# Kernel optimization log

Hardware: AMD Instinct MI355X
Metric: run time of the kernel (lower is better)

## Reference

```python
import jax, jax.numpy as jnp
import numpy as np

N = 50000      # nodes
E = 800000     # edges (before self-loops)
DIN = 64
DH = 64
DOUT = 64
G = 500        # graphs in batch
EPS = 1e-5     # BatchNorm eps


def setup_inputs() -> dict:
    key = jax.random.key(0)
    ks = jax.random.split(key, 8)
    x = jax.random.normal(ks[0], (N, DIN), dtype=jnp.float32)
    edge_index = jax.random.randint(ks[1], (2, E), 0, N, dtype=jnp.int32)
    batch = jnp.sort(jax.random.randint(ks[2], (N,), 0, G, dtype=jnp.int32))

    def lin(k, di, do):
        return (jax.random.normal(k, (di, do), dtype=jnp.float32) / np.float32(np.sqrt(di)))

    inp = dict(x=x, edge_index=edge_index, batch=batch)
    dims = [(DIN, DH), (DH, DH), (DH, DOUT)]
    for i, (di, do) in enumerate(dims, start=1):
        inp[f"W{i}"] = lin(ks[2 + i], di, do)
        inp[f"b{i}"] = jnp.zeros((do,), jnp.float32)
        inp[f"gamma{i}"] = jnp.ones((do,), jnp.float32)
        inp[f"beta{i}"] = jnp.zeros((do,), jnp.float32)
    return inp


def _gcn_norm(edge_index, n_nodes):
    # add self loops, compute symmetric normalization deg^-1/2 * deg^-1/2
    loop = jnp.arange(n_nodes, dtype=edge_index.dtype)
    src = jnp.concatenate([edge_index[0], loop])
    dst = jnp.concatenate([edge_index[1], loop])
    deg = jax.ops.segment_sum(jnp.ones_like(dst, dtype=jnp.float32), dst,
                              num_segments=n_nodes)
    dinv = jax.lax.rsqrt(deg)  # deg >= 1 thanks to self-loops
    norm = dinv[src] * dinv[dst]  # [E + N]
    return src, dst, norm


def _gcn_conv(x, src, dst, norm, W, b, n_nodes):
    h = x @ W                               # [N, dout]
    msg = h[src] * norm[:, None]            # gather + scale  [E+N, dout]
    out = jax.ops.segment_sum(msg, dst, num_segments=n_nodes)  # scatter-add
    return out + b


def _batchnorm(x, gamma, beta):
    mean = jnp.mean(x, axis=0)
    var = jnp.mean(jnp.square(x - mean), axis=0)  # biased, as in torch training BN
    return gamma * (x - mean) * jax.lax.rsqrt(var + EPS) + beta


def reference(x, edge_index, batch, W1, b1, gamma1, beta1,
              W2, b2, gamma2, beta2, W3, b3, gamma3, beta3):
    src, dst, norm = _gcn_norm(edge_index, N)
    layers = [(W1, b1, gamma1, beta1), (W2, b2, gamma2, beta2),
              (W3, b3, gamma3, beta3)]
    h = x
    for i, (W, b, g, be) in enumerate(layers):
        h = _gcn_conv(h, src, dst, norm, W, b, N)
        h = _batchnorm(h, g, be)
        if i < len(layers) - 1:
            h = jax.nn.relu(h)  # dropout is identity in eval / reference
    # global mean pool over graphs
    sums = jax.ops.segment_sum(h, batch, num_segments=G)          # [G, DOUT]
    cnts = jax.ops.segment_sum(jnp.ones((N,), jnp.float32), batch,
                               num_segments=G)
    return sums / jnp.maximum(cnts, 1.0)[:, None]
```

## Files before the change

### kernel.cpp

```cpp
#include <hip/hip_runtime.h>
#include <hip/hip_fp16.h>

#define BN_EPS 1e-5f
#define CCH 4096
#define NSLICE 32
#define OUT_CAP 8192
#define CAP 8192
#define SXS 68


__device__ inline __half2 u2h(unsigned u) {
    union { unsigned u; __half2 h; } x; x.u = u; return x.h;
}
__device__ inline unsigned h2u(__half2 h) {
    union { unsigned u; __half2 h; } x; x.h = h; return x.u;
}
__device__ inline unsigned pack_f16x2(float a, float b) {
    return h2u(__floats2half2_rn(a, b));
}


__global__ __launch_bounds__(256) void scatter_direct(const int* __restrict__ src,
                                                      const int* __restrict__ dst,
                                                      int* __restrict__ ccnt,
                                                      unsigned* __restrict__ tmp,
                                                      float* __restrict__ cnt_g,
                                                      float* __restrict__ out,
                                                      int E, int G) {
    __shared__ int lcnt[256];
    int t = threadIdx.x;
    int tid = blockIdx.x * 256 + t;
    int stride = gridDim.x * 256;
    for (int i = tid; i < G * 64; i += stride) out[i] = 0.f;
    for (int i = tid; i < G; i += stride) cnt_g[i] = 0.f;

    int e0 = blockIdx.x * CCH;
    lcnt[t] = 0;
    __syncthreads();
#pragma unroll
    for (int k = 0; k < CCH / 256; ++k) {
        int e = e0 + k * 256 + t;
        if (e < E) atomicAdd(&lcnt[dst[e] >> 8], 1);
    }
    __syncthreads();
    int c = lcnt[t];
    __syncthreads();
    if (c > 0) lcnt[t] = t * CAP + atomicAdd(&ccnt[t], c);
    __syncthreads();
#pragma unroll
    for (int k = 0; k < CCH / 256; ++k) {
        int e = e0 + k * 256 + t;
        if (e < E) {
            int d = dst[e];
            int pos = atomicAdd(&lcnt[d >> 8], 1);
            tmp[pos] = ((unsigned)src[e] << 8) | (unsigned)(d & 255);
        }
    }
}


__global__ __launch_bounds__(256) void build_csr(const unsigned* __restrict__ tmp,
                                                 const int* __restrict__ ccnt,
                                                 int* __restrict__ rp,
                                                 unsigned short* __restrict__ deg,
                                                 unsigned short* __restrict__ col,
                                                 float* __restrict__ dinv,
                                                 const int* __restrict__ batch,
                                                 float* __restrict__ cnt_g,
                                                 int n, int G) {
    __shared__ int hist[256];
    __shared__ int sc[256];
    __shared__ unsigned short outw[OUT_CAP];
    __shared__ int h[512];
    int b = blockIdx.x;
    int t = threadIdx.x;
    int beg = b * CAP;
    int m = ccnt[b];
    int end = beg + m;
    hist[t] = 0;
    __syncthreads();
    for (int e = beg + t; e < end; e += 256) atomicAdd(&hist[tmp[e] & 255u], 1);
    __syncthreads();
    int v = hist[t];
    sc[t] = v;
    __syncthreads();
    for (int off = 1; off < 256; off <<= 1) {
        int u = (t >= off) ? sc[t - off] : 0;
        __syncthreads();
        sc[t] += u;
        __syncthreads();
    }
    int excl = sc[t] - v;
    int node = b * 256 + t;
    if (node < n) {
        dinv[node] = rsqrtf(1.0f + (float)v);
        rp[node] = beg + excl;
        deg[node] = (unsigned short)v;
    }
    hist[t] = excl;
    __syncthreads();
    if (m <= OUT_CAP) {
        for (int e = beg + t; e < end; e += 256) {
            unsigned p = tmp[e];
            int pos = atomicAdd(&hist[p & 255u], 1);
            outw[pos] = (unsigned short)(p >> 8);
        }
        __syncthreads();
        for (int i = t; i < m; i += 256) col[beg + i] = outw[i];
    } else {
        for (int e = beg + t; e < end; e += 256) {
            unsigned p = tmp[e];
            int pos = atomicAdd(&hist[p & 255u], 1);
            col[beg + pos] = (unsigned short)(p >> 8);
        }
    }
    if (G <= 512) {
        __syncthreads();
        for (int i = t; i < 512; i += 256) h[i] = 0;
        __syncthreads();
        for (int i = b * 256 + t; i < n; i += gridDim.x * 256)
            atomicAdd(&h[batch[i]], 1);
        __syncthreads();
        for (int i = t; i < G; i += 256)
            if (h[i]) atomicAdd(&cnt_g[i], (float)h[i]);
    } else {
        for (int i = b * 256 + t; i < n; i += gridDim.x * 256)
            atomicAdd(&cnt_g[batch[i]], 1.0f);
    }
}


__global__ __launch_bounds__(256) void gemm64_v2(const float* __restrict__ X,
                                                 const float* __restrict__ W,
                                                 const float* __restrict__ dinv,
                                                 const float* __restrict__ part,
                                                 const float* __restrict__ gamma,
                                                 const float* __restrict__ beta,
                                                 int has_bn, float inv_n,
                                                 unsigned* __restrict__ Hs, int n) {
    __shared__ float sX[64 * SXS];
    __shared__ float sW[64 * SXS];
    __shared__ float s_scsh[128];
    int t = threadIdx.x;
    int c4 = t & 15;
    int base = blockIdx.x * 64;

    if (has_bn) {
        if (t < 128) {
            float s = 0.f;
#pragma unroll
            for (int k = 0; k < NSLICE; ++k) s += part[k * 128 + t];
            s_scsh[t] = s;
        }
        __syncthreads();
        if (t < 64) {
            float mean = s_scsh[t] * inv_n;
            float var = s_scsh[64 + t] * inv_n - mean * mean;
            float sc = gamma[t] * rsqrtf(var + BN_EPS);
            s_scsh[t] = sc;
            s_scsh[64 + t] = beta[t] - mean * sc;
        }
        __syncthreads();
    }

    {
        const float4* W4 = (const float4*)W;
#pragma unroll
        for (int it = 0; it < 4; ++it) {
            int idx = it * 256 + t;
            int r = idx >> 4;
            float4 v = W4[r * 16 + c4];
            *(float4*)&sW[r * SXS + c4 * 4] = v;
        }
    }
    {
        const float4* X4 = (const float4*)X;
        float4 sc4, sh4;
        if (has_bn) {
            sc4 = *(const float4*)&s_scsh[c4 * 4];
            sh4 = *(const float4*)&s_scsh[64 + c4 * 4];
        }
#pragma unroll
        for (int it = 0; it < 4; ++it) {
            int idx = it * 256 + t;
            int r = idx >> 4;
            int grow = base + r;
            float4 v = make_float4(0.f, 0.f, 0.f, 0.f);
            if (grow < n) v = X4[(size_t)grow * 16 + c4];
            if (has_bn) {
                v.x = fmaxf(fmaf(v.x, sc4.x, sh4.x), 0.f);
                v.y = fmaxf(fmaf(v.y, sc4.y, sh4.y), 0.f);
                v.z = fmaxf(fmaf(v.z, sc4.z, sh4.z), 0.f);
                v.w = fmaxf(fmaf(v.w, sc4.w, sh4.w), 0.f);
            }
            *(float4*)&sX[r * SXS + c4 * 4] = v;
        }
    }
    __syncthreads();

    int rgrp = t >> 4;
    float4 acc[4];
#pragma unroll
    for (int ri = 0; ri < 4; ++ri) acc[ri] = make_float4(0.f, 0.f, 0.f, 0.f);

#pragma unroll 4
    for (int k4 = 0; k4 < 16; ++k4) {
        float4 xv[4], wv[4];
#pragma unroll
        for (int ri = 0; ri < 4; ++ri)
            xv[ri] = *(const float4*)&sX[(rgrp + 16 * ri) * SXS + k4 * 4];
#pragma unroll
        for (int kk = 0; kk < 4; ++kk)
            wv[kk] = *(const float4*)&sW[(k4 * 4 + kk) * SXS + c4 * 4];
#pragma unroll
        for (int ri = 0; ri < 4; ++ri) {
            acc[ri].x = fmaf(xv[ri].x, wv[0].x, acc[ri].x);
            acc[ri].y = fmaf(xv[ri].x, wv[0].y, acc[ri].y);
            acc[ri].z = fmaf(xv[ri].x, wv[0].z, acc[ri].z);
            acc[ri].w = fmaf(xv[ri].x, wv[0].w, acc[ri].w);
            acc[ri].x = fmaf(xv[ri].y, wv[1].x, acc[ri].x);
            acc[ri].y = fmaf(xv[ri].y, wv[1].y, acc[ri].y);
            acc[ri].z = fmaf(xv[ri].y, wv[1].z, acc[ri].z);
            acc[ri].w = fmaf(xv[ri].y, wv[1].w, acc[ri].w);
            acc[ri].x = fmaf(xv[ri].z, wv[2].x, acc[ri].x);
            acc[ri].y = fmaf(xv[ri].z, wv[2].y, acc[ri].y);
            acc[ri].z = fmaf(xv[ri].z, wv[2].z, acc[ri].z);
            acc[ri].w = fmaf(xv[ri].z, wv[2].w, acc[ri].w);
            acc[ri].x = fmaf(xv[ri].w, wv[3].x, acc[ri].x);
            acc[ri].y = fmaf(xv[ri].w, wv[3].y, acc[ri].y);
            acc[ri].z = fmaf(xv[ri].w, wv[3].z, acc[ri].z);
            acc[ri].w = fmaf(xv[ri].w, wv[3].w, acc[ri].w);
        }
    }

#pragma unroll
    for (int ri = 0; ri < 4; ++ri) {
        int row = base + rgrp + 16 * ri;
        if (row < n) {
            float dv = dinv[row];
            uint2 o2;
            o2.x = pack_f16x2(acc[ri].x * dv, acc[ri].y * dv);
            o2.y = pack_f16x2(acc[ri].z * dv, acc[ri].w * dv);
            ((uint2*)Hs)[(size_t)row * 16 + c4] = o2;
        }
    }
}


__global__ __launch_bounds__(256) void agg(const uint4* __restrict__ Hs4,
                                           const int* __restrict__ rp,
                                           const unsigned short* __restrict__ deg,
                                           const unsigned short* __restrict__ col,
                                           const float* __restrict__ dinv,
                                           float* __restrict__ Y,
                                           float* __restrict__ part, int n) {
    __shared__ float sS[8][64];
    __shared__ float sQ[8][64];
    int t = threadIdx.x;
    int w = t >> 6;
    int lane = t & 63;
    int h = lane >> 5;
    int l5 = lane & 31;
    int g4 = l5 >> 3;
    int c = l5 & 7;
    int d = blockIdx.x * 8 + w * 2 + h;
    bool valid = d < n;
    int dc = valid ? d : 0;
    __half2 a0 = u2h(0u), a1 = u2h(0u), a2 = u2h(0u), a3 = u2h(0u);
    int beg = 0, end = 0;
    if (valid) { beg = rp[dc]; end = beg + (int)deg[dc]; }
    for (int b = beg; b < end; b += 32) {
        int m = min(32, end - b);
        int myidx = (l5 < m) ? (int)col[b + l5] : 0;
        uint4 v[8];
#pragma unroll
        for (int k = 0; k < 8; ++k) {
            int e = 4 * k + g4;
            int s0 = __shfl(myidx, e, 32);
            if (e < m) v[k] = Hs4[(size_t)s0 * 8 + c];
        }
#pragma unroll
        for (int k = 0; k < 8; ++k) {
            int e = 4 * k + g4;
            if (e < m) {
                a0 = __hadd2(a0, u2h(v[k].x)); a1 = __hadd2(a1, u2h(v[k].y));
                a2 = __hadd2(a2, u2h(v[k].z)); a3 = __hadd2(a3, u2h(v[k].w));
            }
        }
    }
#pragma unroll
    for (int mask = 8; mask <= 16; mask <<= 1) {
        a0 = __hadd2(a0, u2h((unsigned)__shfl_xor((int)h2u(a0), mask, 64)));
        a1 = __hadd2(a1, u2h((unsigned)__shfl_xor((int)h2u(a1), mask, 64)));
        a2 = __hadd2(a2, u2h((unsigned)__shfl_xor((int)h2u(a2), mask, 64)));
        a3 = __hadd2(a3, u2h((unsigned)__shfl_xor((int)h2u(a3), mask, 64)));
    }
    if (g4 == 0) {
        float2 f0 = __half22float2(a0), f1 = __half22float2(a1);
        float2 f2 = __half22float2(a2), f3 = __half22float2(a3);
        float y0 = f0.x, y1 = f0.y, y2 = f1.x, y3 = f1.y;
        float y4 = f2.x, y5 = f2.y, y6 = f3.x, y7 = f3.y;
        if (valid) {
            uint4 hv = Hs4[(size_t)dc * 8 + c];
            float2 h0 = __half22float2(u2h(hv.x)), h1 = __half22float2(u2h(hv.y));
            float2 h2v = __half22float2(u2h(hv.z)), h3 = __half22float2(u2h(hv.w));
            float dv = dinv[dc];
            y0 = (y0 + h0.x) * dv; y1 = (y1 + h0.y) * dv;
            y2 = (y2 + h1.x) * dv; y3 = (y3 + h1.y) * dv;
            y4 = (y4 + h2v.x) * dv; y5 = (y5 + h2v.y) * dv;
            y6 = (y6 + h3.x) * dv; y7 = (y7 + h3.y) * dv;
            *(float4*)&Y[(size_t)dc * 64 + c * 8]     = make_float4(y0, y1, y2, y3);
            *(float4*)&Y[(size_t)dc * 64 + c * 8 + 4] = make_float4(y4, y5, y6, y7);
        } else {
            y0 = y1 = y2 = y3 = y4 = y5 = y6 = y7 = 0.f;
        }
        int slot = w * 2 + h;
        *(float4*)&sS[slot][c * 8]     = make_float4(y0, y1, y2, y3);
        *(float4*)&sS[slot][c * 8 + 4] = make_float4(y4, y5, y6, y7);
        *(float4*)&sQ[slot][c * 8]     = make_float4(y0 * y0, y1 * y1, y2 * y2, y3 * y3);
        *(float4*)&sQ[slot][c * 8 + 4] = make_float4(y4 * y4, y5 * y5, y6 * y6, y7 * y7);
    }
    __syncthreads();
    if (t < 64) {
        float s = 0.f, qq = 0.f;
#pragma unroll
        for (int i = 0; i < 8; ++i) { s += sS[i][t]; qq += sQ[i][t]; }
        float* dst = part + (size_t)(blockIdx.x & (NSLICE - 1)) * 128;
        atomicAdd(&dst[t], s);
        atomicAdd(&dst[64 + t], qq);
    }
}

__global__ __launch_bounds__(256) void agg_pool(const uint4* __restrict__ Hs4,
                                                const int* __restrict__ rp,
                                                const unsigned short* __restrict__ deg,
                                                const unsigned short* __restrict__ col,
                                                const float* __restrict__ dinv,
                                                const int* __restrict__ batch,
                                                float* __restrict__ out,
                                                float* __restrict__ part, int n) {
    __shared__ float sS[8][64];
    __shared__ float sQ[8][64];
    __shared__ int sG[8];
    int t = threadIdx.x;
    int w = t >> 6;
    int lane = t & 63;
    int h = lane >> 5;
    int l5 = lane & 31;
    int g4 = l5 >> 3;
    int c = l5 & 7;
    int d = blockIdx.x * 8 + w * 2 + h;
    bool valid = d < n;
    int dc = valid ? d : 0;
    __half2 a0 = u2h(0u), a1 = u2h(0u), a2 = u2h(0u), a3 = u2h(0u);
    int beg = 0, end = 0;
    if (valid) { beg = rp[dc]; end = beg + (int)deg[dc]; }
    for (int b = beg; b < end; b += 32) {
        int m = min(32, end - b);
        int myidx = (l5 < m) ? (int)col[b + l5] : 0;
        uint4 v[8];
#pragma unroll
        for (int k = 0; k < 8; ++k) {
            int e = 4 * k + g4;
            int s0 = __shfl(myidx, e, 32);
            if (e < m) v[k] = Hs4[(size_t)s0 * 8 + c];
        }
#pragma unroll
        for (int k = 0; k < 8; ++k) {
            int e = 4 * k + g4;
            if (e < m) {
                a0 = __hadd2(a0, u2h(v[k].x)); a1 = __hadd2(a1, u2h(v[k].y));
                a2 = __hadd2(a2, u2h(v[k].z)); a3 = __hadd2(a3, u2h(v[k].w));
            }
        }
    }
#pragma unroll
    for (int mask = 8; mask <= 16; mask <<= 1) {
        a0 = __hadd2(a0, u2h((unsigned)__shfl_xor((int)h2u(a0), mask, 64)));
        a1 = __hadd2(a1, u2h((unsigned)__shfl_xor((int)h2u(a1), mask, 64)));
        a2 = __hadd2(a2, u2h((unsigned)__shfl_xor((int)h2u(a2), mask, 64)));
        a3 = __hadd2(a3, u2h((unsigned)__shfl_xor((int)h2u(a3), mask, 64)));
    }
    if (g4 == 0) {
        float2 f0 = __half22float2(a0), f1 = __half22float2(a1);
        float2 f2 = __half22float2(a2), f3 = __half22float2(a3);
        float y0 = f0.x, y1 = f0.y, y2 = f1.x, y3 = f1.y;
        float y4 = f2.x, y5 = f2.y, y6 = f3.x, y7 = f3.y;
        if (valid) {
            uint4 hv = Hs4[(size_t)dc * 8 + c];
            float2 h0 = __half22float2(u2h(hv.x)), h1 = __half22float2(u2h(hv.y));
            float2 h2v = __half22float2(u2h(hv.z)), h3 = __half22float2(u2h(hv.w));
            float dv = dinv[dc];
            y0 = (y0 + h0.x) * dv; y1 = (y1 + h0.y) * dv;
            y2 = (y2 + h1.x) * dv; y3 = (y3 + h1.y) * dv;
            y4 = (y4 + h2v.x) * dv; y5 = (y5 + h2v.y) * dv;
            y6 = (y6 + h3.x) * dv; y7 = (y7 + h3.y) * dv;
        } else {
            y0 = y1 = y2 = y3 = y4 = y5 = y6 = y7 = 0.f;
        }
        int slot = w * 2 + h;
        *(float4*)&sS[slot][c * 8]     = make_float4(y0, y1, y2, y3);
        *(float4*)&sS[slot][c * 8 + 4] = make_float4(y4, y5, y6, y7);
        *(float4*)&sQ[slot][c * 8]     = make_float4(y0 * y0, y1 * y1, y2 * y2, y3 * y3);
        *(float4*)&sQ[slot][c * 8 + 4] = make_float4(y4 * y4, y5 * y5, y6 * y6, y7 * y7);
        if (l5 == 0) sG[slot] = valid ? batch[dc] : -1;
    }
    __syncthreads();
    if (t < 64) {
        float s = 0.f, qq = 0.f;
#pragma unroll
        for (int i = 0; i < 8; ++i) { s += sS[i][t]; qq += sQ[i][t]; }
        float* dst = part + (size_t)(blockIdx.x & (NSLICE - 1)) * 128;
        atomicAdd(&dst[t], s);
        atomicAdd(&dst[64 + t], qq);
        int g0 = sG[0];
        bool same = (g0 >= 0);
#pragma unroll
        for (int i = 1; i < 8; ++i) same = same && (sG[i] == g0);
        if (same) {
            atomicAdd(&out[(size_t)g0 * 64 + t], s);
        } else {
#pragma unroll
            for (int i = 0; i < 8; ++i) {
                int gi = sG[i];
                if (gi >= 0) atomicAdd(&out[(size_t)gi * 64 + t], sS[i][t]);
            }
        }
    }
}


__global__ __launch_bounds__(256) void pool_div(float* __restrict__ out,
                                                const float* __restrict__ cnt,
                                                const float* __restrict__ part,
                                                const float* __restrict__ gamma,
                                                const float* __restrict__ beta,
                                                int G, float inv_n) {
    __shared__ float s_scsh[128];
    int t = threadIdx.x;
    if (t < 128) {
        float s = 0.f;
#pragma unroll
        for (int k = 0; k < NSLICE; ++k) s += part[k * 128 + t];
        s_scsh[t] = s;
    }
    __syncthreads();
    if (t < 64) {
        float mean = s_scsh[t] * inv_n;
        float var = s_scsh[64 + t] * inv_n - mean * mean;
        float sc = gamma[t] * rsqrtf(var + BN_EPS);
        s_scsh[t] = sc;
        s_scsh[64 + t] = beta[t] - mean * sc;
    }
    __syncthreads();
    int idx = blockIdx.x * 256 + t;
    if (idx >= G * 64) return;
    int j = idx & 63, g = idx >> 6;
    float c = cnt[g];
    out[idx] = (c > 0.5f) ? fmaf(s_scsh[j], out[idx] / c, s_scsh[64 + j]) : 0.f;
}


extern "C" void kernel_launch(void* const* d_in, const int* in_sizes, int n_in,
                              void* d_out, int out_size, void* d_ws, size_t ws_size,
                              hipStream_t stream) {
    const float* x     = (const float*)d_in[0];
    const int*   ei    = (const int*)d_in[1];
    const int*   batch = (const int*)d_in[2];
    const float* Wl[3] = {(const float*)d_in[3], (const float*)d_in[7], (const float*)d_in[11]};
    const float* gl[3] = {(const float*)d_in[5], (const float*)d_in[9], (const float*)d_in[13]};
    const float* bl[3] = {(const float*)d_in[6], (const float*)d_in[10], (const float*)d_in[14]};
    float* out = (float*)d_out;

    int E = in_sizes[1] / 2;
    int n = in_sizes[0] / 64;
    int G = out_size / 64;
    const int* src = ei;
    const int* dst = ei + E;
    int NBC = (n + 255) / 256;
    float inv_n = 1.0f / (float)n;

    char* ws = (char*)d_ws;
    size_t off = 0;
    auto carve = [&](size_t bytes) {
        void* p = ws + off;
        off += (bytes + 255) & ~(size_t)255;
        return p;
    };
    float*          part  = (float*)carve(3 * NSLICE * 128 * 4);
    int*            ccnt  = (int*)carve(256 * 4);
    float*          dinv  = (float*)carve((size_t)n * 4);
    float*          cnt_g = (float*)carve((size_t)G * 4);
    unsigned*       Hs    = (unsigned*)carve((size_t)n * 32 * 4);
    float*          Ybuf  = (float*)carve((size_t)n * 64 * 4);
    int*            rp    = (int*)carve(((size_t)n + 1) * 4);
    unsigned short* deg   = (unsigned short*)carve((size_t)n * 2);
    unsigned*       tmp   = (unsigned*)carve((size_t)NBC * CAP * 4);
    unsigned short* col   = (unsigned short*)carve((size_t)NBC * CAP * 2);

    int pgrid = (E + CCH - 1) / CCH;
    int gemm_grid = (n + 63) / 64;
    int agg_grid = (n + 7) / 8;

    hipMemsetAsync(part, 0, 3 * NSLICE * 128 * 4 + 256 * 4, stream);
    scatter_direct<<<pgrid, 256, 0, stream>>>(src, dst, ccnt, tmp, cnt_g, out, E, G);
    build_csr<<<NBC, 256, 0, stream>>>(tmp, ccnt, rp, deg, col, dinv, batch, cnt_g, n, G);

    const float* cur = x;
    for (int l = 0; l < 3; ++l) {
        float* part_l = part + (size_t)l * NSLICE * 128;
        const float* part_prev = (l > 0) ? part + (size_t)(l - 1) * NSLICE * 128 : part;
        gemm64_v2<<<gemm_grid, 256, 0, stream>>>(cur, Wl[l], dinv, part_prev,
                                                 l > 0 ? gl[l - 1] : gl[0],
                                                 l > 0 ? bl[l - 1] : bl[0],
                                                 l > 0 ? 1 : 0, inv_n, Hs, n);
        if (l < 2) {
            agg<<<agg_grid, 256, 0, stream>>>((const uint4*)Hs, rp, deg, col, dinv,
                                              Ybuf, part_l, n);
        } else {
            agg_pool<<<agg_grid, 256, 0, stream>>>((const uint4*)Hs, rp, deg, col, dinv,
                                                   batch, out, part_l, n);
        }
        cur = Ybuf;
    }

    pool_div<<<(G * 64 + 255) / 256, 256, 0, stream>>>(out, cnt_g,
                                                       part + 2 * NSLICE * 128,
                                                       gl[2], bl[2], G, inv_n);
}
```

Before: 229.1 us.

## Assign one 8-lane group per destination node in aggregation kernels

```diff
diff --git a/kernel.cpp b/kernel.cpp
--- a/kernel.cpp
+++ b/kernel.cpp
@@ -254,77 +254,64 @@
                                            const float* __restrict__ dinv,
                                            float* __restrict__ Y,
                                            float* __restrict__ part, int n) {
-    __shared__ float sS[8][64];
-    __shared__ float sQ[8][64];
+    __shared__ float sS[32][64];
+    __shared__ float sQ[32][64];
     int t = threadIdx.x;
     int w = t >> 6;
     int lane = t & 63;
-    int h = lane >> 5;
-    int l5 = lane & 31;
-    int g4 = l5 >> 3;
-    int c = l5 & 7;
-    int d = blockIdx.x * 8 + w * 2 + h;
+    int dslot = lane >> 3;
+    int c = lane & 7;
+    int slot = w * 8 + dslot;
+    int d = blockIdx.x * 32 + slot;
     bool valid = d < n;
     int dc = valid ? d : 0;
     __half2 a0 = u2h(0u), a1 = u2h(0u), a2 = u2h(0u), a3 = u2h(0u);
     int beg = 0, end = 0;
     if (valid) { beg = rp[dc]; end = beg + (int)deg[dc]; }
-    for (int b = beg; b < end; b += 32) {
-        int m = min(32, end - b);
-        int myidx = (l5 < m) ? (int)col[b + l5] : 0;
+    for (int b = beg; b < end; b += 8) {
+        int m = min(8, end - b);
+        int myidx = (c < m) ? (int)col[b + c] : 0;
         uint4 v[8];
 #pragma unroll
         for (int k = 0; k < 8; ++k) {
-            int e = 4 * k + g4;
-            int s0 = __shfl(myidx, e, 32);
-            if (e < m) v[k] = Hs4[(size_t)s0 * 8 + c];
+            int s0 = __shfl(myidx, k, 8);
+            if (k < m) v[k] = Hs4[(size_t)s0 * 8 + c];
         }
 #pragma unroll
         for (int k = 0; k < 8; ++k) {
-            int e = 4 * k + g4;
-            if (e < m) {
+            if (k < m) {
                 a0 = __hadd2(a0, u2h(v[k].x)); a1 = __hadd2(a1, u2h(v[k].y));
                 a2 = __hadd2(a2, u2h(v[k].z)); a3 = __hadd2(a3, u2h(v[k].w));
             }
         }
     }
-#pragma unroll
-    for (int mask = 8; mask <= 16; mask <<= 1) {
-        a0 = __hadd2(a0, u2h((unsigned)__shfl_xor((int)h2u(a0), mask, 64)));
-        a1 = __hadd2(a1, u2h((unsigned)__shfl_xor((int)h2u(a1), mask, 64)));
-        a2 = __hadd2(a2, u2h((unsigned)__shfl_xor((int)h2u(a2), mask, 64)));
-        a3 = __hadd2(a3, u2h((unsigned)__shfl_xor((int)h2u(a3), mask, 64)));
-    }
-    if (g4 == 0) {
-        float2 f0 = __half22float2(a0), f1 = __half22float2(a1);
-        float2 f2 = __half22float2(a2), f3 = __half22float2(a3);
-        float y0 = f0.x, y1 = f0.y, y2 = f1.x, y3 = f1.y;
-        float y4 = f2.x, y5 = f2.y, y6 = f3.x, y7 = f3.y;
-        if (valid) {
-            uint4 hv = Hs4[(size_t)dc * 8 + c];
-            float2 h0 = __half22float2(u2h(hv.x)), h1 = __half22float2(u2h(hv.y));
-            float2 h2v = __half22float2(u2h(hv.z)), h3 = __half22float2(u2h(hv.w));
-            float dv = dinv[dc];
-            y0 = (y0 + h0.x) * dv; y1 = (y1 + h0.y) * dv;
-            y2 = (y2 + h1.x) * dv; y3 = (y3 + h1.y) * dv;
-            y4 = (y4 + h2v.x) * dv; y5 = (y5 + h2v.y) * dv;
-            y6 = (y6 + h3.x) * dv; y7 = (y7 + h3.y) * dv;
-            *(float4*)&Y[(size_t)dc * 64 + c * 8]     = make_float4(y0, y1, y2, y3);
-            *(float4*)&Y[(size_t)dc * 64 + c * 8 + 4] = make_float4(y4, y5, y6, y7);
-        } else {
-            y0 = y1 = y2 = y3 = y4 = y5 = y6 = y7 = 0.f;
-        }
-        int slot = w * 2 + h;
-        *(float4*)&sS[slot][c * 8]     = make_float4(y0, y1, y2, y3);
-        *(float4*)&sS[slot][c * 8 + 4] = make_float4(y4, y5, y6, y7);
-        *(float4*)&sQ[slot][c * 8]     = make_float4(y0 * y0, y1 * y1, y2 * y2, y3 * y3);
-        *(float4*)&sQ[slot][c * 8 + 4] = make_float4(y4 * y4, y5 * y5, y6 * y6, y7 * y7);
-    }
+    float2 f0 = __half22float2(a0), f1 = __half22float2(a1);
+    float2 f2 = __half22float2(a2), f3 = __half22float2(a3);
+    float y0 = f0.x, y1 = f0.y, y2 = f1.x, y3 = f1.y;
+    float y4 = f2.x, y5 = f2.y, y6 = f3.x, y7 = f3.y;
+    if (valid) {
+        uint4 hv = Hs4[(size_t)dc * 8 + c];
+        float2 h0 = __half22float2(u2h(hv.x)), h1 = __half22float2(u2h(hv.y));
+        float2 h2v = __half22float2(u2h(hv.z)), h3 = __half22float2(u2h(hv.w));
+        float dv = dinv[dc];
+        y0 = (y0 + h0.x) * dv; y1 = (y1 + h0.y) * dv;
+        y2 = (y2 + h1.x) * dv; y3 = (y3 + h1.y) * dv;
+        y4 = (y4 + h2v.x) * dv; y5 = (y5 + h2v.y) * dv;
+        y6 = (y6 + h3.x) * dv; y7 = (y7 + h3.y) * dv;
+        *(float4*)&Y[(size_t)dc * 64 + c * 8]     = make_float4(y0, y1, y2, y3);
+        *(float4*)&Y[(size_t)dc * 64 + c * 8 + 4] = make_float4(y4, y5, y6, y7);
+    } else {
+        y0 = y1 = y2 = y3 = y4 = y5 = y6 = y7 = 0.f;
+    }
+    *(float4*)&sS[slot][c * 8]     = make_float4(y0, y1, y2, y3);
+    *(float4*)&sS[slot][c * 8 + 4] = make_float4(y4, y5, y6, y7);
+    *(float4*)&sQ[slot][c * 8]     = make_float4(y0 * y0, y1 * y1, y2 * y2, y3 * y3);
+    *(float4*)&sQ[slot][c * 8 + 4] = make_float4(y4 * y4, y5 * y5, y6 * y6, y7 * y7);
     __syncthreads();
     if (t < 64) {
         float s = 0.f, qq = 0.f;
 #pragma unroll
-        for (int i = 0; i < 8; ++i) { s += sS[i][t]; qq += sQ[i][t]; }
+        for (int i = 0; i < 32; ++i) { s += sS[i][t]; qq += sQ[i][t]; }
         float* dst = part + (size_t)(blockIdx.x & (NSLICE - 1)) * 128;
         atomicAdd(&dst[t], s);
         atomicAdd(&dst[64 + t], qq);
@@ -339,89 +326,76 @@
                                                 const int* __restrict__ batch,
                                                 float* __restrict__ out,
                                                 float* __restrict__ part, int n) {
-    __shared__ float sS[8][64];
-    __shared__ float sQ[8][64];
-    __shared__ int sG[8];
+    __shared__ float sS[32][64];
+    __shared__ float sQ[32][64];
+    __shared__ int sG[32];
     int t = threadIdx.x;
     int w = t >> 6;
     int lane = t & 63;
-    int h = lane >> 5;
-    int l5 = lane & 31;
-    int g4 = l5 >> 3;
-    int c = l5 & 7;
-    int d = blockIdx.x * 8 + w * 2 + h;
+    int dslot = lane >> 3;
+    int c = lane & 7;
+    int slot = w * 8 + dslot;
+    int d = blockIdx.x * 32 + slot;
     bool valid = d < n;
     int dc = valid ? d : 0;
     __half2 a0 = u2h(0u), a1 = u2h(0u), a2 = u2h(0u), a3 = u2h(0u);
     int beg = 0, end = 0;
     if (valid) { beg = rp[dc]; end = beg + (int)deg[dc]; }
-    for (int b = beg; b < end; b += 32) {
-        int m = min(32, end - b);
-        int myidx = (l5 < m) ? (int)col[b + l5] : 0;
+    for (int b = beg; b < end; b += 8) {
+        int m = min(8, end - b);
+        int myidx = (c < m) ? (int)col[b + c] : 0;
         uint4 v[8];
 #pragma unroll
         for (int k = 0; k < 8; ++k) {
-            int e = 4 * k + g4;
-            int s0 = __shfl(myidx, e, 32);
-            if (e < m) v[k] = Hs4[(size_t)s0 * 8 + c];
+            int s0 = __shfl(myidx, k, 8);
+            if (k < m) v[k] = Hs4[(size_t)s0 * 8 + c];
         }
 #pragma unroll
         for (int k = 0; k < 8; ++k) {
-            int e = 4 * k + g4;
-            if (e < m) {
+            if (k < m) {
                 a0 = __hadd2(a0, u2h(v[k].x)); a1 = __hadd2(a1, u2h(v[k].y));
                 a2 = __hadd2(a2, u2h(v[k].z)); a3 = __hadd2(a3, u2h(v[k].w));
             }
         }
     }
-#pragma unroll
-    for (int mask = 8; mask <= 16; mask <<= 1) {
-        a0 = __hadd2(a0, u2h((unsigned)__shfl_xor((int)h2u(a0), mask, 64)));
-        a1 = __hadd2(a1, u2h((unsigned)__shfl_xor((int)h2u(a1), mask, 64)));
-        a2 = __hadd2(a2, u2h((unsigned)__shfl_xor((int)h2u(a2), mask, 64)));
-        a3 = __hadd2(a3, u2h((unsigned)__shfl_xor((int)h2u(a3), mask, 64)));
-    }
-    if (g4 == 0) {
-        float2 f0 = __half22float2(a0), f1 = __half22float2(a1);
-        float2 f2 = __half22float2(a2), f3 = __half22float2(a3);
-        float y0 = f0.x, y1 = f0.y, y2 = f1.x, y3 = f1.y;
-        float y4 = f2.x, y5 = f2.y, y6 = f3.x, y7 = f3.y;
-        if (valid) {
-            uint4 hv = Hs4[(size_t)dc * 8 + c];
-            float2 h0 = __half22float2(u2h(hv.x)), h1 = __half22float2(u2h(hv.y));
-            float2 h2v = __half22float2(u2h(hv.z)), h3 = __half22float2(u2h(hv.w));
-            float dv = dinv[dc];
-            y0 = (y0 + h0.x) * dv; y1 = (y1 + h0.y) * dv;
-            y2 = (y2 + h1.x) * dv; y3 = (y3 + h1.y) * dv;
-            y4 = (y4 + h2v.x) * dv; y5 = (y5 + h2v.y) * dv;
-            y6 = (y6 + h3.x) * dv; y7 = (y7 + h3.y) * dv;
-        } else {
-            y0 = y1 = y2 = y3 = y4 = y5 = y6 = y7 = 0.f;
-        }
-        int slot = w * 2 + h;
-        *(float4*)&sS[slot][c * 8]     = make_float4(y0, y1, y2, y3);
-        *(float4*)&sS[slot][c * 8 + 4] = make_float4(y4, y5, y6, y7);
-        *(float4*)&sQ[slot][c * 8]     = make_float4(y0 * y0, y1 * y1, y2 * y2, y3 * y3);
-        *(float4*)&sQ[slot][c * 8 + 4] = make_float4(y4 * y4, y5 * y5, y6 * y6, y7 * y7);
-        if (l5 == 0) sG[slot] = valid ? batch[dc] : -1;
-    }
+    float2 f0 = __half22float2(a0), f1 = __half22float2(a1);
+    float2 f2 = __half22float2(a2), f3 = __half22float2(a3);
+    float y0 = f0.x, y1 = f0.y, y2 = f1.x, y3 = f1.y;
+    float y4 = f2.x, y5 = f2.y, y6 = f3.x, y7 = f3.y;
+    if (valid) {
+        uint4 hv = Hs4[(size_t)dc * 8 + c];
+        float2 h0 = __half22float2(u2h(hv.x)), h1 = __half22float2(u2h(hv.y));
+        float2 h2v = __half22float2(u2h(hv.z)), h3 = __half22float2(u2h(hv.w));
+        float dv = dinv[dc];
+        y0 = (y0 + h0.x) * dv; y1 = (y1 + h0.y) * dv;
+        y2 = (y2 + h1.x) * dv; y3 = (y3 + h1.y) * dv;
+        y4 = (y4 + h2v.x) * dv; y5 = (y5 + h2v.y) * dv;
+        y6 = (y6 + h3.x) * dv; y7 = (y7 + h3.y) * dv;
+    } else {
+        y0 = y1 = y2 = y3 = y4 = y5 = y6 = y7 = 0.f;
+    }
+    *(float4*)&sS[slot][c * 8]     = make_float4(y0, y1, y2, y3);
+    *(float4*)&sS[slot][c * 8 + 4] = make_float4(y4, y5, y6, y7);
+    *(float4*)&sQ[slot][c * 8]     = make_float4(y0 * y0, y1 * y1, y2 * y2, y3 * y3);
+    *(float4*)&sQ[slot][c * 8 + 4] = make_float4(y4 * y4, y5 * y5, y6 * y6, y7 * y7);
+    if (c == 0) sG[slot] = valid ? batch[dc] : -1;
     __syncthreads();
     if (t < 64) {
         float s = 0.f, qq = 0.f;
 #pragma unroll
-        for (int i = 0; i < 8; ++i) { s += sS[i][t]; qq += sQ[i][t]; }
+        for (int i = 0; i < 32; ++i) { s += sS[i][t]; qq += sQ[i][t]; }
         float* dst = part + (size_t)(blockIdx.x & (NSLICE - 1)) * 128;
         atomicAdd(&dst[t], s);
         atomicAdd(&dst[64 + t], qq);
         int g0 = sG[0];
         bool same = (g0 >= 0);
 #pragma unroll
-        for (int i = 1; i < 8; ++i) same = same && (sG[i] == g0);
+        for (int i = 1; i < 32; ++i) same = same && (sG[i] == g0);
         if (same) {
             atomicAdd(&out[(size_t)g0 * 64 + t], s);
         } else {
 #pragma unroll
-            for (int i = 0; i < 8; ++i) {
+            for (int i = 0; i < 32; ++i) {
                 int gi = sG[i];
                 if (gi >= 0) atomicAdd(&out[(size_t)gi * 64 + t], sS[i][t]);
             }
@@ -500,7 +474,7 @@
 
     int pgrid = (E + CCH - 1) / CCH;
     int gemm_grid = (n + 63) / 64;
-    int agg_grid = (n + 7) / 8;
+    int agg_grid = (n + 31) / 32;
 
     hipMemsetAsync(part, 0, 3 * NSLICE * 128 * 4 + 256 * 4, stream);
     scatter_direct<<<pgrid, 256, 0, stream>>>(src, dst, ccnt, tmp, cnt_g, out, E, G);
```

Result: no change. 229.9 us (+0.3%).
